# Kernel optimization log

Hardware: AMD Instinct MI355X
Metric: run time of the kernel (lower is better)

The kernel has to match this reference:

```python
import jax, jax.numpy as jnp
import numpy as np
from functools import partial

# CUBA leaky integrate-and-fire constants (from the module source)
TH = 0.1            # hidden-layer spike threshold
TH_LAST = 1.0e5     # readout layer: effectively never spikes, voltage is the output
ALPHA_C = 1.0 - 1.0   # current_decay = 1  -> current decay factor 0 (no current memory)
ALPHA_V = 1.0 - 0.01  # voltage_decay = 0.01 -> voltage decay factor 0.99


def heaviside(v, th):
    return (v >= th).astype(v.dtype)


def cuba_dense(x, W, th, spiking=True):
    """Dense synapse + CUBA neuron dynamics.
    x: [B, Cin, T] spikes, W: [Cout, Cin]. Returns spikes (or voltage trace) [B, Cout, T].
    """
    z = jnp.einsum('oi,bit->bot', W, x)   # synapse: per-timestep dense projection
    zT = jnp.moveaxis(z, -1, 0)           # [T, B, Cout] for temporal scan
    state0 = (jnp.zeros(zT.shape[1:], z.dtype), jnp.zeros(zT.shape[1:], z.dtype))

    def step(carry, zt):
        c, v = carry
        c = ALPHA_C * c + zt              # current dynamics
        v = ALPHA_V * v + c               # voltage dynamics
        s = heaviside(v, th)              # spike
        v_next = v * (1.0 - s)            # hard reset to 0 on spike
        out = s if spiking else v
        return (c, v_next), out

    _, out = jax.lax.scan(step, state0, zT)
    return jnp.moveaxis(out, 0, -1)       # [B, Cout, T]


def setup_inputs() -> dict:
    key = jax.random.key(0)
    ks = jax.random.split(key, 5)
    B, T = 32, 300
    C_IN = 34 * 34 * 2  # 2312
    spike = (jax.random.uniform(ks[0], (B, C_IN, T)) < 0.02).astype(jnp.float32)

    def w(k, o, i):
        return jax.random.normal(k, (o, i), jnp.float32) / np.float32(np.sqrt(i))

    return {
        'spike': spike,
        'W1': w(ks[1], 64, C_IN),
        'W2': w(ks[2], 512, 64),
        'W3': w(ks[3], 512, 512),
        'W4': w(ks[4], 10, 512),
    }


def reference(spike, W1, W2, W3, W4):
    s = cuba_dense(spike, W1, TH)
    s = cuba_dense(s, W2, TH)
    s = cuba_dense(s, W3, TH)
    V = cuba_dense(s, W4, TH_LAST, spiking=False)  # neuron.dynamics -> voltage trace
    return V  # [B, 10, T]
```

## Files before the change

kernel.cpp:

```cpp
#include <hip/hip_runtime.h>
#include <hip/hip_bf16.h>

#define ALPHA_V 0.99f
#define TH_HID 0.1f
#define TH_LAST 1.0e5f

static constexpr int B_ = 32, T_ = 300, CIN_ = 2312;
static constexpr int KP1 = 2336;
static constexpr int M_ = 9600;

using short8 = __attribute__((ext_vector_type(8))) short;
using f32x4  = __attribute__((ext_vector_type(4))) float;

__device__ __forceinline__ float bf16bits_to_f(ushort u) {
    union { unsigned int i; float f; } cv; cv.i = ((unsigned int)u) << 16; return cv.f;
}
__device__ __forceinline__ ushort f_to_bf16bits(float f) {
    __hip_bfloat16 h = __float2bfloat16(f);
    return *(ushort*)&h;
}

__global__ void prep_w_all(
    const float* __restrict__ Wa, ushort* __restrict__ WaHi, ushort* __restrict__ WaLo, int Na, int Ka, int Kpa,
    const float* __restrict__ Wb, ushort* __restrict__ WbHi, ushort* __restrict__ WbLo, int Nb, int Kb, int Kpb,
    const float* __restrict__ Wc, ushort* __restrict__ WcHi, ushort* __restrict__ WcLo, int Nc, int Kc, int Kpc)
{
    int idx = blockIdx.x * 256 + threadIdx.x;
    const int ea = Na * Kpa, eb = Nb * Kpb, ec = Nc * Kpc;
    const float* W; ushort *Whi, *Wlo; int K, Kp;
    if (idx < ea) {
        W = Wa; Whi = WaHi; Wlo = WaLo; K = Ka; Kp = Kpa;
    } else if ((idx -= ea) < eb) {
        W = Wb; Whi = WbHi; Wlo = WbLo; K = Kb; Kp = Kpb;
    } else if ((idx -= eb) < ec) {
        W = Wc; Whi = WcHi; Wlo = WcLo; K = Kc; Kp = Kpc;
    } else return;
    int n = idx / Kp, k = idx % Kp;
    float w = (k < K) ? W[(size_t)n * K + k] : 0.f;
    __hip_bfloat16 hi = __float2bfloat16(w);
    float hif = __bfloat162float(hi);
    __hip_bfloat16 lo = __float2bfloat16(w - hif);
    Whi[idx] = *(ushort*)&hi;
    Wlo[idx] = *(ushort*)&lo;
}

__global__ __launch_bounds__(256) void gemm1_fused(
    const float* __restrict__ X, const ushort* __restrict__ Whi,
    const ushort* __restrict__ Wlo, float* __restrict__ P)
{
    constexpr int LP = 40;
    __shared__ ushort As[2][64 * LP];
    __shared__ ushort Bh[2][64 * LP];
    __shared__ ushort Bl[2][64 * LP];

    const int tid = threadIdx.x;
    const int t0 = blockIdx.x * 64;
    const int split = blockIdx.y;
    const int b = blockIdx.z;
    const int stepBeg = split * 19;
    const int nSteps = min(19, 73 - stepBeg);
    const int tvalid = min(64, T_ - t0);
    float* Z = P + (size_t)split * M_ * 64;

    const int wid = tid >> 6, lane = tid & 63;
    const int wm = (wid >> 1) * 32, wn = (wid & 1) * 32;
    const int lr = lane & 15, lk = (lane >> 4) * 8;

    f32x4 acc[2][2];
    {
        f32x4 z4 = {0.f, 0.f, 0.f, 0.f};
        acc[0][0] = z4; acc[0][1] = z4; acc[1][0] = z4; acc[1][1] = z4;
    }

    const int p = tid >> 4;
    const int tq = tid & 15;
    const bool tok = (tq * 4 < tvalid);
    const float* Xb = X + (size_t)b * CIN_ * T_ + t0 + tq * 4;

    const int sr = tid >> 2, sq = (tid & 3) * 8;
    const ushort* Hp = Whi + (size_t)sr * KP1 + (size_t)stepBeg * 32 + sq;
    const ushort* Lp = Wlo + (size_t)sr * KP1 + (size_t)stepBeg * 32 + sq;
    const int sdstW = sr * LP + sq;

    f32x4 xa, xb;
    uint4 rh, rl;

    auto loadStep = [&](int s) {
        int gk = (stepBeg + s) * 32 + 2 * p;
        f32x4 z4 = {0.f, 0.f, 0.f, 0.f};
        xa = z4; xb = z4;
        if (tok) {
            if (gk < CIN_)     xa = *(const f32x4*)&Xb[(size_t)gk * T_];
            if (gk + 1 < CIN_) xb = *(const f32x4*)&Xb[(size_t)(gk + 1) * T_];
        }
        rh = *(const uint4*)(Hp + (size_t)s * 32);
        rl = *(const uint4*)(Lp + (size_t)s * 32);
    };
    auto writeStep = [&](int bufi) {
#pragma unroll
        for (int j = 0; j < 4; ++j) {
            uint u = (uint)f_to_bf16bits(xa[j]) | ((uint)f_to_bf16bits(xb[j]) << 16);
            *(uint*)&As[bufi][(tq * 4 + j) * LP + 2 * p] = u;
        }
        *(uint4*)&Bh[bufi][sdstW] = rh;
        *(uint4*)&Bl[bufi][sdstW] = rl;
    };

    loadStep(0);
    writeStep(0);
    for (int s = 0; s < nSteps; ++s) {
        const int cur = s & 1, nxt = cur ^ 1;
        if (s + 1 < nSteps) loadStep(s + 1);
        __syncthreads();

        short8 af[2], bhf[2], blf[2];
#pragma unroll
        for (int i = 0; i < 2; ++i) {
            af[i]  = *(const short8*)&As[cur][(wm + i * 16 + lr) * LP + lk];
            bhf[i] = *(const short8*)&Bh[cur][(wn + i * 16 + lr) * LP + lk];
            blf[i] = *(const short8*)&Bl[cur][(wn + i * 16 + lr) * LP + lk];
        }
#pragma unroll
        for (int i = 0; i < 2; ++i)
#pragma unroll
            for (int j = 0; j < 2; ++j) {
                acc[i][j] = __builtin_amdgcn_mfma_f32_16x16x32_bf16(af[i], bhf[j], acc[i][j], 0, 0, 0);
                acc[i][j] = __builtin_amdgcn_mfma_f32_16x16x32_bf16(af[i], blf[j], acc[i][j], 0, 0, 0);
            }
        if (s + 1 < nSteps) writeStep(nxt);
    }

    const int orow = (lane >> 4) * 4;
#pragma unroll
    for (int i = 0; i < 2; ++i)
#pragma unroll
        for (int j = 0; j < 2; ++j)
#pragma unroll
            for (int r = 0; r < 4; ++r) {
                int tl = wm + i * 16 + orow + r;
                if (tl < tvalid)
                    Z[(size_t)(b * T_ + t0 + tl) * 64 + (wn + j * 16 + lr)] = acc[i][j][r];
            }
}

__global__ __launch_bounds__(256) void gemm_mfma64(
    const ushort* __restrict__ A, const ushort* __restrict__ Whi,
    const ushort* __restrict__ Wlo, float* __restrict__ Z,
    int lda, int ldz, int nSteps)
{
    constexpr int LP = 40;
    __shared__ ushort As[2][64 * LP];
    __shared__ ushort Bh[2][64 * LP];
    __shared__ ushort Bl[2][64 * LP];

    const int tid = threadIdx.x;
    const int m0 = blockIdx.x * 64, n0 = blockIdx.y * 64;

    const int wid = tid >> 6, lane = tid & 63;
    const int wm = (wid >> 1) * 32, wn = (wid & 1) * 32;
    const int lr = lane & 15, lk = (lane >> 4) * 8;

    f32x4 acc[2][2];
    {
        f32x4 z4 = {0.f, 0.f, 0.f, 0.f};
        acc[0][0] = z4; acc[0][1] = z4; acc[1][0] = z4; acc[1][1] = z4;
    }

    const int sr = tid >> 2, sq = (tid & 3) * 8;
    const ushort* Ap = A   + (size_t)(m0 + sr) * lda + sq;
    const ushort* Hp = Whi + (size_t)(n0 + sr) * lda + sq;
    const ushort* Lp = Wlo + (size_t)(n0 + sr) * lda + sq;
    const int sdst = sr * LP + sq;

    uint4 ra = *(const uint4*)(Ap);
    uint4 rh = *(const uint4*)(Hp);
    uint4 rl = *(const uint4*)(Lp);
    *(uint4*)&As[0][sdst] = ra;
    *(uint4*)&Bh[0][sdst] = rh;
    *(uint4*)&Bl[0][sdst] = rl;

    for (int s = 0; s < nSteps; ++s) {
        const int cur = s & 1, nxt = cur ^ 1;
        if (s + 1 < nSteps) {
            ra = *(const uint4*)(Ap + (size_t)(s + 1) * 32);
            rh = *(const uint4*)(Hp + (size_t)(s + 1) * 32);
            rl = *(const uint4*)(Lp + (size_t)(s + 1) * 32);
        }
        __syncthreads();

        short8 af[2], bhf[2], blf[2];
#pragma unroll
        for (int i = 0; i < 2; ++i) {
            af[i]  = *(const short8*)&As[cur][(wm + i * 16 + lr) * LP + lk];
            bhf[i] = *(const short8*)&Bh[cur][(wn + i * 16 + lr) * LP + lk];
            blf[i] = *(const short8*)&Bl[cur][(wn + i * 16 + lr) * LP + lk];
        }
#pragma unroll
        for (int i = 0; i < 2; ++i)
#pragma unroll
            for (int j = 0; j < 2; ++j) {
                acc[i][j] = __builtin_amdgcn_mfma_f32_16x16x32_bf16(af[i], bhf[j], acc[i][j], 0, 0, 0);
                acc[i][j] = __builtin_amdgcn_mfma_f32_16x16x32_bf16(af[i], blf[j], acc[i][j], 0, 0, 0);
            }
        if (s + 1 < nSteps) {
            *(uint4*)&As[nxt][sdst] = ra;
            *(uint4*)&Bh[nxt][sdst] = rh;
            *(uint4*)&Bl[nxt][sdst] = rl;
        }
    }

    const int orow = (lane >> 4) * 4;
#pragma unroll
    for (int i = 0; i < 2; ++i)
#pragma unroll
        for (int j = 0; j < 2; ++j)
#pragma unroll
            for (int r = 0; r < 4; ++r)
                Z[(size_t)(m0 + wm + i * 16 + orow + r) * ldz + (n0 + wn + j * 16 + lr)]
                    = acc[i][j][r];
}

#define LOADC(buf, t0)                                                       \
    _Pragma("unroll")                                                        \
    for (int j = 0; j < CH; ++j) {                                           \
        float sacc = zp[(size_t)((t0) + j) * C];                             \
        _Pragma("unroll")                                                    \
        for (int k = 1; k < NS; ++k)                                         \
            sacc += zp[(size_t)k * splitStride + (size_t)((t0) + j) * C];    \
        buf[j] = sacc;                                                       \
    }
#define SCANC(buf, t0)                                                       \
    _Pragma("unroll")                                                        \
    for (int j = 0; j < CH; ++j) {                                           \
        v = ALPHA_V * v + buf[j];                                            \
        bool sp = (v >= th);                                                 \
        op[(size_t)((t0) + j) * C] = sp ? (ushort)0x3F80 : (ushort)0;        \
        v = sp ? 0.f : v;                                                    \
    }

template<int NS, int CH>
__global__ __launch_bounds__(64) void scan_tpn2(
    const float* __restrict__ z, ushort* __restrict__ out,
    int shiftC, size_t splitStride, float th)
{
    const int C = 1 << shiftC;
    const int idx = blockIdx.x * 64 + threadIdx.x;
    if (idx >= B_ * C) return;
    const int b = idx >> shiftC, c = idx & (C - 1);
    const float* zp = z + (size_t)b * T_ * C + c;
    ushort* op = out + (size_t)b * T_ * C + c;

    float va[CH], vb[CH];
    float v = 0.f;
    constexpr int NCH = T_ / CH;
    static_assert(T_ % CH == 0, "chunk must divide T");

    LOADC(va, 0)
    for (int ch = 0; ch < NCH; ch += 2) {
        if (ch + 1 < NCH) { LOADC(vb, (ch + 1) * CH) }
        SCANC(va, ch * CH)
        if (ch + 2 < NCH) { LOADC(va, (ch + 2) * CH) }
        if (ch + 1 < NCH) { SCANC(vb, (ch + 1) * CH) }
    }
}
#undef LOADC
#undef SCANC

__global__ __launch_bounds__(256) void gemm4_kernel(
    const ushort* __restrict__ S, const float* __restrict__ W4,
    float* __restrict__ out)
{
    __shared__ float W4s[10 * 512];
    for (int e = threadIdx.x; e < 5120; e += 256) W4s[e] = W4[e];
    __syncthreads();

    const int wid = (blockIdx.x * 256 + threadIdx.x) >> 6;
    const int l = threadIdx.x & 63;
    const int b = wid / T_, t = wid % T_;

    const ushort* Srow = S + (size_t)wid * 512;
    float acc[10] = {};
#pragma unroll
    for (int j = 0; j < 2; ++j) {
        ushort4 sv = *(const ushort4*)&Srow[j * 256 + l * 4];
        float s0 = bf16bits_to_f(sv.x), s1 = bf16bits_to_f(sv.y),
              s2 = bf16bits_to_f(sv.z), s3 = bf16bits_to_f(sv.w);
#pragma unroll
        for (int o = 0; o < 10; ++o) {
            float4 wv = *(const float4*)&W4s[o * 512 + j * 256 + l * 4];
            acc[o] += s0 * wv.x + s1 * wv.y + s2 * wv.z + s3 * wv.w;
        }
    }
#pragma unroll
    for (int o = 0; o < 10; ++o) {
        float v = acc[o];
        v += __shfl_xor(v, 32); v += __shfl_xor(v, 16); v += __shfl_xor(v, 8);
        v += __shfl_xor(v, 4);  v += __shfl_xor(v, 2);  v += __shfl_xor(v, 1);
        if (l == 0) out[((size_t)b * 10 + o) * T_ + t] = v;
    }
}

__global__ void scan4_tpn(float* __restrict__ out)
{
    int idx = blockIdx.x * 64 + threadIdx.x;
    if (idx >= B_ * 10) return;
    float* p = out + (size_t)idx * T_;
    float v = 0.f;
#pragma unroll 4
    for (int t = 0; t < T_; ++t) {
        v = ALPHA_V * v + p[t];
        p[t] = v;
        if (v >= TH_LAST) v = 0.f;
    }
}

extern "C" void kernel_launch(void* const* d_in, const int* in_sizes, int n_in,
                              void* d_out, int out_size, void* d_ws, size_t ws_size,
                              hipStream_t stream) {
    const float* spike = (const float*)d_in[0];
    const float* W1 = (const float*)d_in[1];
    const float* W2 = (const float*)d_in[2];
    const float* W3 = (const float*)d_in[3];
    const float* W4 = (const float*)d_in[4];
    float* out = (float*)d_out;

    char* ws = (char*)d_ws;
    float*  P  = (float*)ws;
    ushort* S1 = (ushort*)(ws + 9830400);
    float*  Zf = (float*)(ws + 11059200);
    ushort* S2 = (ushort*)(ws + 30720000);
    ushort* S3 = (ushort*)(ws + 40550400);
    ushort* W1hi = (ushort*)(ws + 50380800);
    ushort* W1lo = W1hi + (size_t)64 * KP1;
    ushort* W2hi = W1lo + (size_t)64 * KP1;
    ushort* W2lo = W2hi + (size_t)512 * 64;
    ushort* W3hi = W2lo + (size_t)512 * 64;
    ushort* W3lo = W3hi + (size_t)512 * 512;

    const int prepElems = 64 * KP1 + 512 * 64 + 512 * 512;
    prep_w_all<<<(prepElems + 255) / 256, 256, 0, stream>>>(
        W1, W1hi, W1lo, 64, CIN_, KP1,
        W2, W2hi, W2lo, 512, 64, 64,
        W3, W3hi, W3lo, 512, 512, 512);

    gemm1_fused<<<dim3(5, 4, 32), 256, 0, stream>>>(spike, W1hi, W1lo, P);
    scan_tpn2<4, 10><<<(B_ * 64 + 63) / 64, 64, 0, stream>>>(
        P, S1, 6, (size_t)M_ * 64, TH_HID);

    gemm_mfma64<<<dim3(150, 8), 256, 0, stream>>>(S1, W2hi, W2lo, Zf, 64, 512, 2);
    scan_tpn2<1, 10><<<(B_ * 512 + 63) / 64, 64, 0, stream>>>(
        Zf, S2, 9, 0, TH_HID);

    gemm_mfma64<<<dim3(150, 8), 256, 0, stream>>>(S2, W3hi, W3lo, Zf, 512, 512, 16);
    scan_tpn2<1, 10><<<(B_ * 512 + 63) / 64, 64, 0, stream>>>(
        Zf, S3, 9, 0, TH_HID);

    gemm4_kernel<<<2400, 256, 0, stream>>>(S3, W4, out);
    scan4_tpn<<<5, 64, 0, stream>>>(out);
}
```

Measured before the change: 146.9 us.

## Fuse layer-2/3 GEMM with LIF scan in one kernel per layer

Replaces the separate GEMM and scan kernels for hidden layers 2 and 3 with one templated kernel per layer. Each block keeps a 64-output slice of the hi/lo weights resident in LDS and walks one batch's timesteps in 64-row tiles. It computes the tile with MFMA, stages the results in shared memory, and has 64 threads advance the voltage recurrence serially and write spikes. This removes the float Z intermediate round-trip through global memory and two kernel launches. In exchange it uses a large LDS footprint (about one block per CU) and runs the serial scan after each GEMM tile with no overlap.

```diff
diff --git a/kernel.cpp b/kernel.cpp
--- a/kernel.cpp
+++ b/kernel.cpp
@@ -143,81 +143,106 @@
             }
 }
 
-__global__ __launch_bounds__(256) void gemm_mfma64(
-    const ushort* __restrict__ A, const ushort* __restrict__ Whi,
-    const ushort* __restrict__ Wlo, float* __restrict__ Z,
-    int lda, int ldz, int nSteps)
-{
-    constexpr int LP = 40;
-    __shared__ ushort As[2][64 * LP];
-    __shared__ ushort Bh[2][64 * LP];
-    __shared__ ushort Bl[2][64 * LP];
+template<int K>
+__global__ __launch_bounds__(256) void fused_layer(
+    const ushort* __restrict__ Sin, const ushort* __restrict__ Whi,
+    const ushort* __restrict__ Wlo, ushort* __restrict__ Sout, float th)
+{
+    constexpr int WLP = K + 2;
+    constexpr int ALP = 34;
+    constexpr int NSTEP = K / 32;
+    constexpr int TOTSTEP = 5 * NSTEP;
+    __shared__ ushort WhL[64 * WLP];
+    __shared__ ushort WlL[64 * WLP];
+    __shared__ ushort AsL[64 * ALP];
+    __shared__ float  Zl[64][65];
 
     const int tid = threadIdx.x;
-    const int m0 = blockIdx.x * 64, n0 = blockIdx.y * 64;
+    const int o0 = blockIdx.x * 64;
+    const int b  = blockIdx.y;
+
+    constexpr int SEGS = K / 8;
+    for (int e = tid; e < 64 * SEGS; e += 256) {
+        int row = e / SEGS, seg = e % SEGS;
+        *(uint4*)&WhL[row * WLP + seg * 8] = *(const uint4*)&Whi[(size_t)(o0 + row) * K + seg * 8];
+        *(uint4*)&WlL[row * WLP + seg * 8] = *(const uint4*)&Wlo[(size_t)(o0 + row) * K + seg * 8];
+    }
 
     const int wid = tid >> 6, lane = tid & 63;
     const int wm = (wid >> 1) * 32, wn = (wid & 1) * 32;
     const int lr = lane & 15, lk = (lane >> 4) * 8;
-
-    f32x4 acc[2][2];
-    {
-        f32x4 z4 = {0.f, 0.f, 0.f, 0.f};
-        acc[0][0] = z4; acc[0][1] = z4; acc[1][0] = z4; acc[1][1] = z4;
-    }
+    const int orow = (lane >> 4) * 4;
 
     const int sr = tid >> 2, sq = (tid & 3) * 8;
-    const ushort* Ap = A   + (size_t)(m0 + sr) * lda + sq;
-    const ushort* Hp = Whi + (size_t)(n0 + sr) * lda + sq;
-    const ushort* Lp = Wlo + (size_t)(n0 + sr) * lda + sq;
-    const int sdst = sr * LP + sq;
-
-    uint4 ra = *(const uint4*)(Ap);
-    uint4 rh = *(const uint4*)(Hp);
-    uint4 rl = *(const uint4*)(Lp);
-    *(uint4*)&As[0][sdst] = ra;
-    *(uint4*)&Bh[0][sdst] = rh;
-    *(uint4*)&Bl[0][sdst] = rl;
-
-    for (int s = 0; s < nSteps; ++s) {
-        const int cur = s & 1, nxt = cur ^ 1;
-        if (s + 1 < nSteps) {
-            ra = *(const uint4*)(Ap + (size_t)(s + 1) * 32);
-            rh = *(const uint4*)(Hp + (size_t)(s + 1) * 32);
-            rl = *(const uint4*)(Lp + (size_t)(s + 1) * 32);
-        }
+    const ushort* Ab = Sin + (size_t)b * T_ * K;
+
+    float v = 0.f;
+
+    uint4 ra;
+    auto loadChunk = [&](int g) {
+        int tt = g / NSTEP, s = g - tt * NSTEP;
+        int trow = tt * 64 + sr;
+        if (trow < T_) ra = *(const uint4*)&Ab[(size_t)trow * K + s * 32 + sq];
+        else           ra = make_uint4(0u, 0u, 0u, 0u);
+    };
+    loadChunk(0);
+    __syncthreads();
+
+    for (int tt = 0; tt < 5; ++tt) {
+        const int tvalid = min(64, T_ - tt * 64);
+        f32x4 acc[2][2];
+        {
+            f32x4 z4 = {0.f, 0.f, 0.f, 0.f};
+            acc[0][0] = z4; acc[0][1] = z4; acc[1][0] = z4; acc[1][1] = z4;
+        }
+        for (int s = 0; s < NSTEP; ++s) {
+            *(uint4*)&AsL[sr * ALP + sq] = ra;
+            int g = tt * NSTEP + s + 1;
+            if (g < TOTSTEP) loadChunk(g);
+            __syncthreads();
+
+            short8 af[2], bh[2], bl[2];
+#pragma unroll
+            for (int i = 0; i < 2; ++i)
+                af[i] = *(const short8*)&AsL[(wm + i * 16 + lr) * ALP + lk];
+#pragma unroll
+            for (int j = 0; j < 2; ++j) {
+                bh[j] = *(const short8*)&WhL[(wn + j * 16 + lr) * WLP + s * 32 + lk];
+                bl[j] = *(const short8*)&WlL[(wn + j * 16 + lr) * WLP + s * 32 + lk];
+            }
+#pragma unroll
+            for (int i = 0; i < 2; ++i)
+#pragma unroll
+                for (int j = 0; j < 2; ++j) {
+                    acc[i][j] = __builtin_amdgcn_mfma_f32_16x16x32_bf16(af[i], bh[j], acc[i][j], 0, 0, 0);
+                    acc[i][j] = __builtin_amdgcn_mfma_f32_16x16x32_bf16(af[i], bl[j], acc[i][j], 0, 0, 0);
+                }
+            __syncthreads();
+        }
+#pragma unroll
+        for (int i = 0; i < 2; ++i)
+#pragma unroll
+            for (int j = 0; j < 2; ++j)
+#pragma unroll
+                for (int r = 0; r < 4; ++r)
+                    Zl[wm + i * 16 + orow + r][wn + j * 16 + lr] = acc[i][j][r];
         __syncthreads();
 
-        short8 af[2], bhf[2], blf[2];
-#pragma unroll
-        for (int i = 0; i < 2; ++i) {
-            af[i]  = *(const short8*)&As[cur][(wm + i * 16 + lr) * LP + lk];
-            bhf[i] = *(const short8*)&Bh[cur][(wn + i * 16 + lr) * LP + lk];
-            blf[i] = *(const short8*)&Bl[cur][(wn + i * 16 + lr) * LP + lk];
-        }
-#pragma unroll
-        for (int i = 0; i < 2; ++i)
-#pragma unroll
-            for (int j = 0; j < 2; ++j) {
-                acc[i][j] = __builtin_amdgcn_mfma_f32_16x16x32_bf16(af[i], bhf[j], acc[i][j], 0, 0, 0);
-                acc[i][j] = __builtin_amdgcn_mfma_f32_16x16x32_bf16(af[i], blf[j], acc[i][j], 0, 0, 0);
+        if (tid < 64) {
+            float vv = v;
+            ushort* op = Sout + ((size_t)(b * T_ + tt * 64)) * 512 + o0 + tid;
+#pragma unroll 4
+            for (int t = 0; t < tvalid; ++t) {
+                float z = Zl[t][tid];
+                vv = ALPHA_V * vv + z;
+                bool sp = (vv >= th);
+                op[(size_t)t * 512] = sp ? (ushort)0x3F80 : (ushort)0;
+                vv = sp ? 0.f : vv;
             }
-        if (s + 1 < nSteps) {
-            *(uint4*)&As[nxt][sdst] = ra;
-            *(uint4*)&Bh[nxt][sdst] = rh;
-            *(uint4*)&Bl[nxt][sdst] = rl;
-        }
-    }
-
-    const int orow = (lane >> 4) * 4;
-#pragma unroll
-    for (int i = 0; i < 2; ++i)
-#pragma unroll
-        for (int j = 0; j < 2; ++j)
-#pragma unroll
-            for (int r = 0; r < 4; ++r)
-                Z[(size_t)(m0 + wm + i * 16 + orow + r) * ldz + (n0 + wn + j * 16 + lr)]
-                    = acc[i][j][r];
+            v = vv;
+        }
+        __syncthreads();
+    }
 }
 
 #define LOADC(buf, t0)                                                       \
@@ -327,10 +352,9 @@
     char* ws = (char*)d_ws;
     float*  P  = (float*)ws;
     ushort* S1 = (ushort*)(ws + 9830400);
-    float*  Zf = (float*)(ws + 11059200);
-    ushort* S2 = (ushort*)(ws + 30720000);
-    ushort* S3 = (ushort*)(ws + 40550400);
-    ushort* W1hi = (ushort*)(ws + 50380800);
+    ushort* S2 = (ushort*)(ws + 11059200);
+    ushort* S3 = (ushort*)(ws + 20889600);
+    ushort* W1hi = (ushort*)(ws + 30720000);
     ushort* W1lo = W1hi + (size_t)64 * KP1;
     ushort* W2hi = W1lo + (size_t)64 * KP1;
     ushort* W2lo = W2hi + (size_t)512 * 64;
@@ -347,13 +371,9 @@
     scan_tpn2<4, 10><<<(B_ * 64 + 63) / 64, 64, 0, stream>>>(
         P, S1, 6, (size_t)M_ * 64, TH_HID);
 
-    gemm_mfma64<<<dim3(150, 8), 256, 0, stream>>>(S1, W2hi, W2lo, Zf, 64, 512, 2);
-    scan_tpn2<1, 10><<<(B_ * 512 + 63) / 64, 64, 0, stream>>>(
-        Zf, S2, 9, 0, TH_HID);
-
-    gemm_mfma64<<<dim3(150, 8), 256, 0, stream>>>(S2, W3hi, W3lo, Zf, 512, 512, 16);
-    scan_tpn2<1, 10><<<(B_ * 512 + 63) / 64, 64, 0, stream>>>(
-        Zf, S3, 9, 0, TH_HID);
+    fused_layer<64><<<dim3(8, 32), 256, 0, stream>>>(S1, W2hi, W2lo, S2, TH_HID);
+
+    fused_layer<512><<<dim3(8, 32), 256, 0, stream>>>(S2, W3hi, W3lo, S3, TH_HID);
 
     gemm4_kernel<<<2400, 256, 0, stream>>>(S3, W4, out);
     scan4_tpn<<<5, 64, 0, stream>>>(out);
```

Result: slower. 154.8 us (+5.4%).
